# Performance work log

Measured on AMD Instinct MI355X. Metric: run time of the kernel, lower is better.

The kernel has to match this reference:

```python
import jax, jax.numpy as jnp
import numpy as np

EPS = 1e-5
GROUPS = 32

def group_norm(x, w, b):
    B, C, H, W = x.shape
    g = GROUPS
    xr = x.reshape(B, g, C // g, H * W)
    mean = xr.mean(axis=(2, 3), keepdims=True)
    var = xr.var(axis=(2, 3), keepdims=True)
    h = ((xr - mean) / jnp.sqrt(var + EPS)).reshape(B, C, H, W)
    return h * w[None, :, None, None] + b[None, :, None, None]

def setup_inputs() -> dict:
    key = jax.random.key(0)
    ks = jax.random.split(key, 7)
    B, C, H, W = 8, 256, 64, 64
    d = C // 8  # 32
    x = jax.random.normal(ks[0], (B, C, H, W), dtype=jnp.float32)
    norm_w = 1.0 + 0.1 * jax.random.normal(ks[1], (C,), dtype=jnp.float32)
    norm_b = 0.1 * jax.random.normal(ks[2], (C,), dtype=jnp.float32)
    s = 1.0 / np.sqrt(C)
    Wq = jax.random.normal(ks[3], (d, C), dtype=jnp.float32) * s
    Wk = jax.random.normal(ks[4], (d, C), dtype=jnp.float32) * s
    Wv = jax.random.normal(ks[5], (C, C), dtype=jnp.float32) * s
    Wproj = jax.random.normal(ks[6], (C, C), dtype=jnp.float32) * s
    gamma = jnp.full((1,), 0.5, dtype=jnp.float32)  # torch init is 0; nonzero so attention path contributes
    return {"x": x, "norm_w": norm_w, "norm_b": norm_b, "Wq": Wq, "Wk": Wk,
            "Wv": Wv, "Wproj": Wproj, "gamma": gamma}

def reference(x, norm_w, norm_b, Wq, Wk, Wv, Wproj, gamma):
    B, C, H, W = x.shape
    N = H * W
    h = group_norm(x, norm_w, norm_b)           # (B,C,H,W)
    hf = h.reshape(B, C, N)                      # flatten spatial
    d = Wq.shape[0]
    q = jnp.einsum('dc,bcn->bnd', Wq, hf)        # (B,N,d)
    k = jnp.einsum('dc,bcn->bdn', Wk, hf)        # (B,d,N)
    v = jnp.einsum('oc,bcn->bno', Wv, hf)        # (B,N,C)
    scale = d ** (-0.5)
    attn = jax.nn.softmax(jnp.einsum('bnd,bdm->bnm', q, k) * scale, axis=-1)  # (B,N,N)
    out = jnp.einsum('bnm,bmo->bno', attn, v)    # (B,N,C)
    out = out.transpose(0, 2, 1).reshape(B, C, H, W)
    proj = jnp.einsum('oc,bchw->bohw', Wproj, out)
    return x + gamma[0] * proj
```

## Files before the change

### kernel.cpp

```cpp
#include <hip/hip_runtime.h>
#include <cstdint>


typedef __bf16 bf16x8 __attribute__((ext_vector_type(8)));
typedef float f32x4 __attribute__((ext_vector_type(4)));
typedef float f32x16 __attribute__((ext_vector_type(16)));
typedef unsigned int u32x4 __attribute__((ext_vector_type(4)));
typedef unsigned short u16x4 __attribute__((ext_vector_type(4)));
typedef unsigned short u16x8 __attribute__((ext_vector_type(8)));

#define DEVI __device__ __forceinline__

DEVI unsigned short f2bf(float f) {
    __bf16 h = (__bf16)f;
    return __builtin_bit_cast(unsigned short, h);
}
DEVI float bf2f(unsigned short u) {
    unsigned int x = ((unsigned int)u) << 16;
    return __builtin_bit_cast(float, x);
}

DEVI f32x4 mfma16(bf16x8 a, bf16x8 b, f32x4 c) {
    return __builtin_amdgcn_mfma_f32_16x16x32_bf16(a, b, c, 0, 0, 0);
}
DEVI f32x16 mfma32(bf16x8 a, bf16x8 b, f32x16 c) {
    return __builtin_amdgcn_mfma_f32_32x32x16_bf16(a, b, c, 0, 0, 0);
}

DEVI void glds16(const unsigned short* g, unsigned short* l) {
    const __attribute__((address_space(1))) unsigned int* gp =
        reinterpret_cast<const __attribute__((address_space(1))) unsigned int*>(
            reinterpret_cast<uintptr_t>(g));
    __attribute__((address_space(3))) unsigned int* lp =
        reinterpret_cast<__attribute__((address_space(3))) unsigned int*>(
            reinterpret_cast<uintptr_t>(l));
    __builtin_amdgcn_global_load_lds(gp, lp, 16, 0, 0);
}

DEVI void barrier_raw() {
    asm volatile("" ::: "memory");
    __builtin_amdgcn_s_barrier();
    asm volatile("" ::: "memory");
}
DEVI void wait_vm0() {
    __builtin_amdgcn_s_waitcnt(0x3F70);
}

#define QSCALE 0.2550663133f
#define MFIX   12.0f

__global__ __launch_bounds__(256) void k_pack(
        const float* __restrict__ wq, const float* __restrict__ wk,
        const float* __restrict__ wv, const float* __restrict__ wp,
        unsigned short* __restrict__ bqk, unsigned short* __restrict__ bv,
        unsigned short* __restrict__ bp) {
    int i = blockIdx.x * 256 + threadIdx.x;
    if (i < 8192)       bqk[i] = f2bf(wq[i] * QSCALE);
    else if (i < 16384) bqk[i] = f2bf(wk[i - 8192]);
    bv[i] = f2bf(wv[i]);
    bp[i] = f2bf(wp[i]);
}

__global__ __launch_bounds__(1024) void k_gnorm(
        const float* __restrict__ x, const float* __restrict__ gw,
        const float* __restrict__ gb, unsigned short* __restrict__ ht) {
    int bg = blockIdx.x;
    int b = bg >> 5, g = bg & 31;
    const float* xb = x + ((size_t)(b * 256 + g * 8)) * 4096;
    int t = threadIdx.x;
    float s1 = 0.f, s2 = 0.f;
    const f32x4* xv4 = (const f32x4*)xb;
    for (int i = t; i < 8192; i += 1024) {
        f32x4 v = xv4[i];
        #pragma unroll
        for (int j = 0; j < 4; j++) { s1 += v[j]; s2 += v[j] * v[j]; }
    }
    #pragma unroll
    for (int off = 1; off < 64; off <<= 1) {
        s1 += __shfl_xor(s1, off);
        s2 += __shfl_xor(s2, off);
    }
    __shared__ float red[34];
    int wv_ = t >> 6;
    if ((t & 63) == 0) { red[wv_ * 2] = s1; red[wv_ * 2 + 1] = s2; }
    __syncthreads();
    if (t == 0) {
        float a = 0.f, q = 0.f;
        #pragma unroll
        for (int i = 0; i < 16; i++) { a += red[i * 2]; q += red[i * 2 + 1]; }
        float mean = a * (1.f / 32768.f);
        float var = q * (1.f / 32768.f) - mean * mean;
        red[32] = mean; red[33] = rsqrtf(var + 1e-5f);
    }
    __syncthreads();
    float mean = red[32], rstd = red[33];
    float wv8[8], bv8[8];
    #pragma unroll
    for (int c = 0; c < 8; c++) { wv8[c] = gw[g * 8 + c] * rstd; bv8[c] = gb[g * 8 + c] - mean * rstd * gw[g * 8 + c]; }
    int n0 = t * 4;
    f32x4 cv[8];
    #pragma unroll
    for (int c = 0; c < 8; c++) cv[c] = *(const f32x4*)(xb + c * 4096 + n0);
    #pragma unroll
    for (int j = 0; j < 4; j++) {
        u16x8 pk;
        #pragma unroll
        for (int c = 0; c < 8; c++) pk[c] = f2bf(cv[c][j] * wv8[c] + bv8[c]);
        *(u16x8*)(&ht[((size_t)(b * 4096 + n0 + j)) * 256 + g * 8]) = pk;
    }
}

template <int EPI>
__global__ __launch_bounds__(256) void k_gemm(
        const unsigned short* __restrict__ A, const unsigned short* __restrict__ Bw,
        void* __restrict__ outp, const float* __restrict__ xres,
        const float* __restrict__ gamma, int ldout) {
    __shared__ unsigned short lA[128 * 72];
    __shared__ unsigned short lB[64 * 72];
    int t = threadIdx.x;
    int m0 = blockIdx.x * 128, n0 = blockIdx.y * 64;
    int w = t >> 6, lane = t & 63, l15 = lane & 15, quad = lane >> 4;
    f32x4 z4 = {0.f, 0.f, 0.f, 0.f};
    f32x4 acc[2][4];
    #pragma unroll
    for (int i = 0; i < 2; i++)
        #pragma unroll
        for (int j = 0; j < 4; j++) acc[i][j] = z4;

    for (int kb = 0; kb < 4; kb++) {
        #pragma unroll
        for (int i = 0; i < 4; i++) {
            int ch = i * 256 + t;
            int row = ch >> 3, col = (ch & 7) * 8;
            u32x4 v = *(const u32x4*)(A + (size_t)(m0 + row) * 256 + kb * 64 + col);
            *(u32x4*)(&lA[row * 72 + col]) = v;
        }
        #pragma unroll
        for (int i = 0; i < 2; i++) {
            int ch = i * 256 + t;
            int row = ch >> 3, col = (ch & 7) * 8;
            u32x4 v = *(const u32x4*)(Bw + (size_t)(n0 + row) * 256 + kb * 64 + col);
            *(u32x4*)(&lB[row * 72 + col]) = v;
        }
        __syncthreads();
        #pragma unroll
        for (int ks = 0; ks < 2; ks++) {
            bf16x8 af[2], bfr[4];
            #pragma unroll
            for (int fr = 0; fr < 2; fr++)
                af[fr] = *(const bf16x8*)(&lA[(w * 32 + fr * 16 + l15) * 72 + ks * 32 + quad * 8]);
            #pragma unroll
            for (int fn = 0; fn < 4; fn++)
                bfr[fn] = *(const bf16x8*)(&lB[(fn * 16 + l15) * 72 + ks * 32 + quad * 8]);
            #pragma unroll
            for (int fr = 0; fr < 2; fr++)
                #pragma unroll
                for (int fn = 0; fn < 4; fn++)
                    acc[fr][fn] = mfma16(af[fr], bfr[fn], acc[fr][fn]);
        }
        __syncthreads();
    }

    if (EPI == 0) {
        unsigned short* out = (unsigned short*)outp;
        #pragma unroll
        for (int fr = 0; fr < 2; fr++)
            #pragma unroll
            for (int fn = 0; fn < 4; fn++)
                #pragma unroll
                for (int r = 0; r < 4; r++) {
                    int m = m0 + w * 32 + fr * 16 + quad * 4 + r;
                    int n = n0 + fn * 16 + l15;
                    out[(size_t)m * ldout + n] = f2bf(acc[fr][fn][r]);
                }
    } else if (EPI == 1) {
        unsigned short* out = (unsigned short*)outp;
        int b = m0 >> 12, nb = (m0 & 4095) + w * 32;
        int swq = ((quad & 1) << 1) | (quad >> 1);
        #pragma unroll
        for (int fr = 0; fr < 2; fr++)
            #pragma unroll
            for (int fn = 0; fn < 4; fn++) {
                int o = n0 + fn * 16 + l15;
                int n = nb + fr * 16 + swq * 4;
                u16x4 pk;
                #pragma unroll
                for (int r = 0; r < 4; r++) pk[r] = f2bf(acc[fr][fn][r]);
                *(u16x4*)(&out[(((size_t)(b * 256 + o)) << 12) + n]) = pk;
            }
    } else {
        float* out = (float*)outp;
        float gm = gamma[0];
        int b = m0 >> 12, nb = (m0 & 4095) + w * 32;
        #pragma unroll
        for (int fr = 0; fr < 2; fr++)
            #pragma unroll
            for (int fn = 0; fn < 4; fn++) {
                int o = n0 + fn * 16 + l15;
                int n = nb + fr * 16 + quad * 4;
                size_t base = (((size_t)(b * 256 + o)) << 12) + n;
                f32x4 xv = *(const f32x4*)(xres + base);
                f32x4 ov;
                #pragma unroll
                for (int r = 0; r < 4; r++) ov[r] = xv[r] + gm * acc[fr][fn][r];
                *(f32x4*)(out + base) = ov;
            }
    }
}

__global__ __launch_bounds__(256, 2) void k_flash(
        const unsigned short* __restrict__ QK, const unsigned short* __restrict__ Vt,
        unsigned short* __restrict__ Oa) {
    __shared__ __align__(16) char smem[40960];
    int id = blockIdx.x;
    int b = id & 7;
    int r3 = id >> 3;
    int oh = r3 & 1, qblk = r3 >> 1;
    int t = threadIdx.x, w = t >> 6, ln = t & 63;
    int l31 = ln & 31, h = ln >> 5;
    int qh = w >> 1, kh = w & 1;
    int q0 = qblk * 128 + qh * 64;

    bf16x8 qb0[2], qb1[2];
    #pragma unroll
    for (int qt2 = 0; qt2 < 2; qt2++) {
        const unsigned short* qrow = QK + ((size_t)(b * 4096 + q0 + qt2 * 32 + l31)) * 64;
        qb0[qt2] = *(const bf16x8*)(qrow + h * 8);
        qb1[qt2] = *(const bf16x8*)(qrow + 16 + h * 8);
    }

    int cgK = (ln & 3) ^ ((ln >> 2) & 3) ^ ((ln >> 4) & 3);
    const unsigned short* gK = QK + ((size_t)(b * 4096 + w * 16 + (ln >> 2))) * 64 + 32 + cgK * 8;
    int vc8 = (ln & 7) ^ ((ln >> 3) & 7);
    const unsigned short* gV = Vt + (((size_t)(b * 256 + oh * 128 + w * 32 + (ln >> 3))) << 12) + vc8 * 8;

    unsigned short* lK0 = (unsigned short*)smem;
    unsigned short* lV0 = (unsigned short*)(smem + 4096);
    unsigned short* lK1 = (unsigned short*)(smem + 20480);
    unsigned short* lV1 = (unsigned short*)(smem + 24576);
    unsigned short* sK0 = lK0 + w * 512;
    unsigned short* sV0 = lV0 + w * 2048;
    unsigned short* sK1 = lK1 + w * 512;
    unsigned short* sV1 = lV1 + w * 2048;

    f32x16 z16;
    #pragma unroll
    for (int i = 0; i < 16; i++) z16[i] = 0.f;
    f32x16 minit;
    #pragma unroll
    for (int i = 0; i < 16; i++) minit[i] = -MFIX;
    f32x16 Oacc[2][4];
    #pragma unroll
    for (int qt2 = 0; qt2 < 2; qt2++)
        #pragma unroll
        for (int i = 0; i < 4; i++) Oacc[qt2][i] = z16;
    float lsum[2] = {0.f, 0.f};

    int gl = (l31 & 3) ^ ((l31 >> 2) & 3);
    const unsigned short* kf0p0 = lK0 + (kh * 32 + l31) * 32 + ((0 + h) ^ gl) * 8;
    const unsigned short* kf1p0 = lK0 + (kh * 32 + l31) * 32 + ((2 + h) ^ gl) * 8;
    const unsigned short* kf0p1 = lK1 + (kh * 32 + l31) * 32 + ((0 + h) ^ gl) * 8;
    const unsigned short* kf1p1 = lK1 + (kh * 32 + l31) * 32 + ((2 + h) ^ gl) * 8;
    int slotA = ((kh * 4 + 0 * 2 + h) ^ (ln & 7)) * 8;
    int slotB = ((kh * 4 + 1 * 2 + h) ^ (ln & 7)) * 8;

    auto stage = [&](int kn, unsigned short* sK, unsigned short* sV) {
        glds16(gK + (size_t)kn * 4096, sK);
        #pragma unroll
        for (int j = 0; j < 4; j++)
            glds16(gV + ((size_t)j * 8 << 12) + kn * 64, sV + j * 512);
    };

    auto compute = [&](const unsigned short* kf0p, const unsigned short* kf1p,
                       const unsigned short* lV) {
        bf16x8 kf0 = *(const bf16x8*)kf0p;
        bf16x8 kf1 = *(const bf16x8*)kf1p;
        bf16x8 pa[2][2];
        #pragma unroll
        for (int qt2 = 0; qt2 < 2; qt2++) {
            f32x16 St = mfma32(kf0, qb0[qt2], minit);
            St = mfma32(kf1, qb1[qt2], St);
            u16x8 p0u, p1u;
            float s = 0.f;
            #pragma unroll
            for (int j = 0; j < 8; j++) {
                float e0 = __builtin_amdgcn_exp2f(St[j]);
                float e1 = __builtin_amdgcn_exp2f(St[8 + j]);
                s += e0 + e1;
                p0u[j] = f2bf(e0);
                p1u[j] = f2bf(e1);
            }
            lsum[qt2] += s;
            pa[qt2][0] = __builtin_bit_cast(bf16x8, p0u);
            pa[qt2][1] = __builtin_bit_cast(bf16x8, p1u);
        }
        #pragma unroll
        for (int nt = 0; nt < 4; nt++) {
            bf16x8 vf = *(const bf16x8*)(lV + (nt * 32 + l31) * 64 + slotA);
            Oacc[0][nt] = mfma32(pa[0][0], vf, Oacc[0][nt]);
            Oacc[1][nt] = mfma32(pa[1][0], vf, Oacc[1][nt]);
        }
        #pragma unroll
        for (int nt = 0; nt < 4; nt++) {
            bf16x8 vf = *(const bf16x8*)(lV + (nt * 32 + l31) * 64 + slotB);
            Oacc[0][nt] = mfma32(pa[0][1], vf, Oacc[0][nt]);
            Oacc[1][nt] = mfma32(pa[1][1], vf, Oacc[1][nt]);
        }
    };

    stage(0, sK0, sV0);
    for (int kt = 0; kt < 64; kt += 2) {
        wait_vm0();
        barrier_raw();
        stage(kt + 1, sK1, sV1);
        compute(kf0p0, kf1p0, lV0);
        wait_vm0();
        barrier_raw();
        if (kt + 2 < 64) stage(kt + 2, sK0, sV0);
        compute(kf0p1, kf1p1, lV1);
    }
    #pragma unroll
    for (int qt2 = 0; qt2 < 2; qt2++) lsum[qt2] += __shfl_xor(lsum[qt2], 32);
    __syncthreads();

    float* sf = (float*)smem;
    int lbase = (kh ? 8192 : 8320) + qh * 64 + l31;
    sf[lbase] = lsum[0];
    sf[lbase + 32] = lsum[1];
    if (kh == 1) {
        #pragma unroll
        for (int qt2 = 0; qt2 < 2; qt2++)
            #pragma unroll
            for (int nt = 0; nt < 4; nt++)
                #pragma unroll
                for (int rg = 0; rg < 2; rg++) {
                    u16x8 pk;
                    #pragma unroll
                    for (int j = 0; j < 8; j++) pk[j] = f2bf(Oacc[qt2][nt][rg * 8 + j]);
                    *(u16x8*)(smem + qh * 16384 + qt2 * 8192 + nt * 2048 + rg * 1024 + ln * 16) = pk;
                }
    }
    __syncthreads();
    if (kh == 0) {
        #pragma unroll
        for (int qt2 = 0; qt2 < 2; qt2++) {
            float rl[16];
            #pragma unroll
            for (int r = 0; r < 16; r++) {
                int row = (r & 3) + 8 * (r >> 2) + 4 * h;
                float l = sf[8192 + qh * 64 + qt2 * 32 + row] +
                          sf[8320 + qh * 64 + qt2 * 32 + row];
                rl[r] = 1.f / l;
            }
            size_t rb = (size_t)(b * 4096 + qblk * 128 + qh * 64 + qt2 * 32);
            #pragma unroll
            for (int nt = 0; nt < 4; nt++)
                #pragma unroll
                for (int rg = 0; rg < 2; rg++) {
                    u16x8 pk = *(const u16x8*)(smem + qh * 16384 + qt2 * 8192 + nt * 2048 + rg * 1024 + ln * 16);
                    #pragma unroll
                    for (int j = 0; j < 8; j++) {
                        int r = rg * 8 + j;
                        float val = (Oacc[qt2][nt][r] + bf2f(pk[j])) * rl[r];
                        int row = (r & 3) + 8 * (r >> 2) + 4 * h;
                        Oa[(rb + row) * 256 + oh * 128 + nt * 32 + l31] = f2bf(val);
                    }
                }
        }
    }
}

extern "C" void kernel_launch(void* const* d_in, const int* in_sizes, int n_in,
                              void* d_out, int out_size, void* d_ws, size_t ws_size,
                              hipStream_t stream) {
    const float* x  = (const float*)d_in[0];
    const float* nw = (const float*)d_in[1];
    const float* nb = (const float*)d_in[2];
    const float* wq = (const float*)d_in[3];
    const float* wk = (const float*)d_in[4];
    const float* wv = (const float*)d_in[5];
    const float* wp = (const float*)d_in[6];
    const float* gm = (const float*)d_in[7];

    char* p = (char*)d_ws;
    unsigned short* ht  = (unsigned short*)p; p += (size_t)32768 * 256 * 2;
    unsigned short* qk  = (unsigned short*)p; p += (size_t)32768 * 64 * 2;
    unsigned short* vt  = (unsigned short*)p; p += (size_t)8 * 256 * 4096 * 2;
    unsigned short* oa  = (unsigned short*)p; p += (size_t)32768 * 256 * 2;
    unsigned short* bqk = (unsigned short*)p; p += 64 * 256 * 2;
    unsigned short* bv  = (unsigned short*)p; p += 256 * 256 * 2;
    unsigned short* bp  = (unsigned short*)p; p += 256 * 256 * 2;

    k_pack<<<dim3(256), dim3(256), 0, stream>>>(wq, wk, wv, wp, bqk, bv, bp);
    k_gnorm<<<dim3(256), dim3(1024), 0, stream>>>(x, nw, nb, ht);
    k_gemm<0><<<dim3(256, 1), dim3(256), 0, stream>>>(ht, bqk, (void*)qk, nullptr, nullptr, 64);
    k_gemm<1><<<dim3(256, 4), dim3(256), 0, stream>>>(ht, bv, (void*)vt, nullptr, nullptr, 0);
    k_flash<<<dim3(512), dim3(256), 0, stream>>>(qk, vt, oa);
    k_gemm<2><<<dim3(256, 4), dim3(256), 0, stream>>>(oa, bp, d_out, x, gm, 0);
}
```

Before: 232.0 us.

## Merge QK and V projection GEMMs, single-pass groupnorm loads, prioritize PV MFMAs

Three changes. The QK and V projection GEMMs become one launch with a 5-wide grid, where blockIdx.y selects the weight matrix and the epilogue. The group-norm kernel now loads its 8 channel vectors once into registers and computes the statistics from them, instead of reading x twice. The flash kernel raises wave priority around the PV MFMA block. Together these aim to cut one launch and tail, halve the group-norm global reads, and improve MFMA issue, at the cost of some branching in the GEMM.

```diff
diff --git a/kernel.cpp b/kernel.cpp
--- a/kernel.cpp
+++ b/kernel.cpp
@@ -68,12 +68,15 @@
     int b = bg >> 5, g = bg & 31;
     const float* xb = x + ((size_t)(b * 256 + g * 8)) * 4096;
     int t = threadIdx.x;
+    int n0 = t * 4;
+    f32x4 cv[8];
+    #pragma unroll
+    for (int c = 0; c < 8; c++) cv[c] = *(const f32x4*)(xb + c * 4096 + n0);
     float s1 = 0.f, s2 = 0.f;
-    const f32x4* xv4 = (const f32x4*)xb;
-    for (int i = t; i < 8192; i += 1024) {
-        f32x4 v = xv4[i];
-        #pragma unroll
-        for (int j = 0; j < 4; j++) { s1 += v[j]; s2 += v[j] * v[j]; }
+    #pragma unroll
+    for (int c = 0; c < 8; c++) {
+        #pragma unroll
+        for (int j = 0; j < 4; j++) { s1 += cv[c][j]; s2 += cv[c][j] * cv[c][j]; }
     }
     #pragma unroll
     for (int off = 1; off < 64; off <<= 1) {
@@ -97,10 +100,6 @@
     float wv8[8], bv8[8];
     #pragma unroll
     for (int c = 0; c < 8; c++) { wv8[c] = gw[g * 8 + c] * rstd; bv8[c] = gb[g * 8 + c] - mean * rstd * gw[g * 8 + c]; }
-    int n0 = t * 4;
-    f32x4 cv[8];
-    #pragma unroll
-    for (int c = 0; c < 8; c++) cv[c] = *(const f32x4*)(xb + c * 4096 + n0);
     #pragma unroll
     for (int j = 0; j < 4; j++) {
         u16x8 pk;
@@ -114,11 +113,17 @@
 __global__ __launch_bounds__(256) void k_gemm(
         const unsigned short* __restrict__ A, const unsigned short* __restrict__ Bw,
         void* __restrict__ outp, const float* __restrict__ xres,
-        const float* __restrict__ gamma, int ldout) {
+        const float* __restrict__ gamma, int ldout,
+        const unsigned short* __restrict__ Bw2, void* __restrict__ outp2) {
     __shared__ unsigned short lA[128 * 72];
     __shared__ unsigned short lB[64 * 72];
     int t = threadIdx.x;
     int m0 = blockIdx.x * 128, n0 = blockIdx.y * 64;
+    const unsigned short* Bsrc = Bw;
+    if (EPI == 3) {
+        if (blockIdx.y == 0) { n0 = 0; }
+        else { Bsrc = Bw2; n0 = (blockIdx.y - 1) * 64; }
+    }
     int w = t >> 6, lane = t & 63, l15 = lane & 15, quad = lane >> 4;
     f32x4 z4 = {0.f, 0.f, 0.f, 0.f};
     f32x4 acc[2][4];
@@ -139,7 +144,7 @@
         for (int i = 0; i < 2; i++) {
             int ch = i * 256 + t;
             int row = ch >> 3, col = (ch & 7) * 8;
-            u32x4 v = *(const u32x4*)(Bw + (size_t)(n0 + row) * 256 + kb * 64 + col);
+            u32x4 v = *(const u32x4*)(Bsrc + (size_t)(n0 + row) * 256 + kb * 64 + col);
             *(u32x4*)(&lB[row * 72 + col]) = v;
         }
         __syncthreads();
@@ -161,7 +166,9 @@
         __syncthreads();
     }
 
-    if (EPI == 0) {
+    bool epi0 = (EPI == 0) || (EPI == 3 && blockIdx.y == 0);
+    bool epi1 = (EPI == 1) || (EPI == 3 && blockIdx.y != 0);
+    if (epi0) {
         unsigned short* out = (unsigned short*)outp;
         #pragma unroll
         for (int fr = 0; fr < 2; fr++)
@@ -173,8 +180,8 @@
                     int n = n0 + fn * 16 + l15;
                     out[(size_t)m * ldout + n] = f2bf(acc[fr][fn][r]);
                 }
-    } else if (EPI == 1) {
-        unsigned short* out = (unsigned short*)outp;
+    } else if (epi1) {
+        unsigned short* out = (unsigned short*)((EPI == 3) ? outp2 : outp);
         int b = m0 >> 12, nb = (m0 & 4095) + w * 32;
         int swq = ((quad & 1) << 1) | (quad >> 1);
         #pragma unroll
@@ -294,6 +301,7 @@
             pa[qt2][0] = __builtin_bit_cast(bf16x8, p0u);
             pa[qt2][1] = __builtin_bit_cast(bf16x8, p1u);
         }
+        __builtin_amdgcn_s_setprio(1);
         #pragma unroll
         for (int nt = 0; nt < 4; nt++) {
             bf16x8 vf = *(const bf16x8*)(lV + (nt * 32 + l31) * 64 + slotA);
@@ -306,6 +314,7 @@
             Oacc[0][nt] = mfma32(pa[0][1], vf, Oacc[0][nt]);
             Oacc[1][nt] = mfma32(pa[1][1], vf, Oacc[1][nt]);
         }
+        __builtin_amdgcn_s_setprio(0);
     };
 
     stage(0, sK0, sV0);
@@ -393,8 +402,7 @@
 
     k_pack<<<dim3(256), dim3(256), 0, stream>>>(wq, wk, wv, wp, bqk, bv, bp);
     k_gnorm<<<dim3(256), dim3(1024), 0, stream>>>(x, nw, nb, ht);
-    k_gemm<0><<<dim3(256, 1), dim3(256), 0, stream>>>(ht, bqk, (void*)qk, nullptr, nullptr, 64);
-    k_gemm<1><<<dim3(256, 4), dim3(256), 0, stream>>>(ht, bv, (void*)vt, nullptr, nullptr, 0);
+    k_gemm<3><<<dim3(256, 5), dim3(256), 0, stream>>>(ht, bqk, (void*)qk, nullptr, nullptr, 64, bv, (void*)vt);
     k_flash<<<dim3(512), dim3(256), 0, stream>>>(qk, vt, oa);
-    k_gemm<2><<<dim3(256, 4), dim3(256), 0, stream>>>(oa, bp, d_out, x, gm, 0);
-}
+    k_gemm<2><<<dim3(256, 4), dim3(256), 0, stream>>>(oa, bp, d_out, x, gm, 0, nullptr, nullptr);
+}
```

New measurement: 225.3 us. -2.9%, faster.
